# Kernel optimization log

Measured on AMD Instinct MI355X. Metric: run time of the kernel, lower is better.

Reference implementation:

```python
import jax, jax.numpy as jnp
import numpy as np

FILTER_1D = [1.0, 3.0, 3.0, 1.0]  # StyleGAN2 default resample filter
UP = 2


def make_kernel():
    f = jnp.array(FILTER_1D, dtype=jnp.float32)
    k = jnp.outer(f, f)
    k = k / jnp.sum(k)  # setup_filter normalization
    return k * (UP * UP)  # * 4 gain registered in the module


def setup_inputs() -> dict:
    key = jax.random.key(0)
    x = jax.random.normal(key, (4, 64, 256, 256), dtype=jnp.float32)
    return {"x": x, "kernel": make_kernel()}


def reference(x, kernel):
    # upfirdn2d(x, kernel, up=2): zero-insert upsample by 2, pad (fw+up-1)//2=2
    # before and (fw-up)//2=1 after, then FIR-convolve (true convolution ->
    # flip kernel; the [1,3,3,1] kernel is symmetric so this is a no-op, but
    # we flip for faithfulness). Implemented as a single depthwise dilated conv
    # so the padded/upsampled intermediate is never materialized.
    N, C, H, W = x.shape
    w = jnp.flip(kernel)[None, None, :, :].astype(x.dtype)  # [1,1,4,4]
    w = jnp.tile(w, (C, 1, 1, 1))  # depthwise weight [C,1,4,4]
    out = jax.lax.conv_general_dilated(
        x, w,
        window_strides=(1, 1),
        padding=((2, 1), (2, 1)),
        lhs_dilation=(UP, UP),
        dimension_numbers=("NCHW", "OIHW", "NCHW"),
        feature_group_count=C,
    )  # [N, C, 2H, 2W]
    return out
```

## Files before the change

kernel.cpp:

```cpp
#include <hip/hip_runtime.h>
#include <math.h>


template<int S>
__device__ __forceinline__ void hblend(float v0, float v1, float vm1,
                                       float vp0, float vp1, float q[4]) {
    if (S == 0) {
        q[0] = 0.25f*vm1 + 0.75f*v0;
        q[1] = 0.75f*v0  + 0.25f*v1;
        q[2] = 0.25f*v0  + 0.75f*v1;
        q[3] = 0.75f*v1  + 0.25f*vp0;
    } else if (S == 1) {
        q[0] = 0.75f*v0  + 0.25f*v1;
        q[1] = 0.25f*v0  + 0.75f*v1;
        q[2] = 0.75f*v1  + 0.25f*vp0;
        q[3] = 0.25f*v1  + 0.75f*vp0;
    } else if (S == 2) {
        q[0] = 0.25f*v0  + 0.75f*v1;
        q[1] = 0.75f*v1  + 0.25f*vp0;
        q[2] = 0.25f*v1  + 0.75f*vp0;
        q[3] = 0.75f*vp0 + 0.25f*vp1;
    } else {
        q[0] = 0.75f*v1  + 0.25f*vp0;
        q[1] = 0.25f*v1  + 0.75f*vp0;
        q[2] = 0.75f*vp0 + 0.25f*vp1;
        q[3] = 0.25f*vp0 + 0.75f*vp1;
    }
}

template<int S>
__device__ __forceinline__ void store_row(float* __restrict__ rp, int lane,
                                          int Wo, const float q1[4],
                                          const float q2[4],
                                          float v0lane, float v1lane) {
    *(float4*)(rp + S + 4 * lane) = make_float4(q1[0], q1[1], q1[2], q1[3]);
    int c0 = S + 256 + 4 * lane;
    if (c0 + 3 < Wo) {
        *(float4*)(rp + c0) = make_float4(q2[0], q2[1], q2[2], q2[3]);
    } else {
        if (c0     < Wo) rp[c0]     = q2[0];
        if (c0 + 1 < Wo) rp[c0 + 1] = q2[1];
        if (c0 + 2 < Wo) rp[c0 + 2] = q2[2];
        if (c0 + 3 < Wo) rp[c0 + 3] = q2[3];
    }
    if (S > 0 && lane == 0) {
        rp[0] = 0.75f * v0lane;
        if (S > 1) rp[1] = 0.75f * v0lane + 0.25f * v1lane;
        if (S > 2) rp[2] = 0.25f * v0lane + 0.75f * v1lane;
    }
}

template<int SE>
__device__ __forceinline__ void row_pair(
    const float* __restrict__ xp, float* __restrict__ out, size_t be,
    int lane, int i, int H, int W, int Ho, int Wo) {
    constexpr int SO = (SE + 1) & 3;
    int im = i > 0 ? i - 1 : 0;
    int ip = i < H - 1 ? i + 1 : H - 1;
    const float2* ra = (const float2*)(xp + im * W);
    const float2* rb = (const float2*)(xp + i  * W);
    const float2* rc = (const float2*)(xp + ip * W);
    float2 a1 = ra[lane],      b1 = rb[lane],      c1 = rc[lane];
    float2 a2 = ra[64 + lane], b2 = rb[64 + lane], c2 = rc[64 + lane];
    float w0 = (i > 0)     ? 0.25f : 0.0f;
    float wp = (i < H - 1) ? 0.25f : 0.0f;

    float ve10 = w0*a1.x + 0.75f*b1.x, ve11 = w0*a1.y + 0.75f*b1.y;
    float ve20 = w0*a2.x + 0.75f*b2.x, ve21 = w0*a2.y + 0.75f*b2.y;
    float vo10 = 0.75f*b1.x + wp*c1.x, vo11 = 0.75f*b1.y + wp*c1.y;
    float vo20 = 0.75f*b2.x + wp*c2.x, vo21 = 0.75f*b2.y + wp*c2.y;

    float t;
    float vm1e1 = __shfl_up(ve11, 1);   if (lane == 0)  vm1e1 = 0.f;
    float vp0e1 = __shfl_down(ve10, 1);
    t = __shfl(ve20, 0);                if (lane == 63) vp0e1 = t;
    float vp1e1 = __shfl_down(ve11, 1);
    t = __shfl(ve21, 0);                if (lane == 63) vp1e1 = t;
    float vm1e2 = __shfl_up(ve21, 1);
    t = __shfl(ve11, 63);               if (lane == 0)  vm1e2 = t;
    float vp0e2 = __shfl_down(ve20, 1); if (lane == 63) vp0e2 = 0.f;
    float vp1e2 = __shfl_down(ve21, 1); if (lane == 63) vp1e2 = 0.f;
    float vm1o1 = __shfl_up(vo11, 1);   if (lane == 0)  vm1o1 = 0.f;
    float vp0o1 = __shfl_down(vo10, 1);
    t = __shfl(vo20, 0);                if (lane == 63) vp0o1 = t;
    float vp1o1 = __shfl_down(vo11, 1);
    t = __shfl(vo21, 0);                if (lane == 63) vp1o1 = t;
    float vm1o2 = __shfl_up(vo21, 1);
    t = __shfl(vo11, 63);               if (lane == 0)  vm1o2 = t;
    float vp0o2 = __shfl_down(vo20, 1); if (lane == 63) vp0o2 = 0.f;
    float vp1o2 = __shfl_down(vo21, 1); if (lane == 63) vp1o2 = 0.f;

    float q1[4], q2[4];
    float* re = out + be;
    hblend<SE>(ve10, ve11, vm1e1, vp0e1, vp1e1, q1);
    hblend<SE>(ve20, ve21, vm1e2, vp0e2, vp1e2, q2);
    store_row<SE>(re, lane, Wo, q1, q2, ve10, ve11);

    if (2 * i + 1 < Ho) {
        float* ro = re + Wo;
        hblend<SO>(vo10, vo11, vm1o1, vp0o1, vp1o1, q1);
        hblend<SO>(vo20, vo21, vm1o2, vp0o2, vp1o2, q2);
        store_row<SO>(ro, lane, Wo, q1, q2, vo10, vo11);
    }
}

__global__ __launch_bounds__(256) void blur_up2_kernel(
    const float* __restrict__ x, float* __restrict__ out,
    int H, int W, int Ho, int Wo) {
    int lane = threadIdx.x;
    int i = blockIdx.y * 4 + threadIdx.y;
    int nc = blockIdx.z;
    if (i >= H) return;

    const float* xp = x + (size_t)nc * H * W;
    size_t be = (size_t)nc * Ho * Wo + (size_t)(2 * i) * Wo;
    int S = (int)((4 - (be & 3)) & 3);
    switch (S) {
        case 0:  row_pair<0>(xp, out, be, lane, i, H, W, Ho, Wo); break;
        case 1:  row_pair<1>(xp, out, be, lane, i, H, W, Ho, Wo); break;
        case 2:  row_pair<2>(xp, out, be, lane, i, H, W, Ho, Wo); break;
        default: row_pair<3>(xp, out, be, lane, i, H, W, Ho, Wo); break;
    }
}

extern "C" void kernel_launch(void* const* d_in, const int* in_sizes, int n_in,
                              void* d_out, int out_size, void* d_ws, size_t ws_size,
                              hipStream_t stream) {
    const float* x = (const float*)d_in[0];
    float* out = (float*)d_out;

    const int H = 256, W = 256;
    int NC = in_sizes[0] / (H * W);

    int hw_out = out_size / NC;
    int Wo = (int)(sqrt((double)hw_out) + 0.5);
    int Ho = hw_out / Wo;

    dim3 block(64, 4);
    dim3 grid(1, (H + 3) / 4, NC);
    blur_up2_kernel<<<grid, block, 0, stream>>>(x, out, H, W, Ho, Wo);
}
```

Measured before the change: 80.43 us.

## Process two input rows per thread and use nontemporal output stores

Each wavefront now handles two adjacent input rows, loading four input rows once and sharing the middle two between both output row pairs, which cuts redundant input reads from three to two rows per input row. The grid is halved to 32 row-blocks, and all output writes switch to nontemporal stores so the write-only output stream bypasses cache retention. The trade-off is fewer, heavier threads, which may reduce latency hiding. The grid size is now hardcoded for H=256.

Measured after the change: 82.96 us. 1.03x slower.

```diff
diff --git a/kernel.cpp b/kernel.cpp
--- a/kernel.cpp
+++ b/kernel.cpp
@@ -1,6 +1,8 @@
 #include <hip/hip_runtime.h>
 #include <math.h>
 
+
+typedef float vfloat4 __attribute__((ext_vector_type(4)));
 
 template<int S>
 __device__ __forceinline__ void hblend(float v0, float v1, float vm1,
@@ -33,37 +35,31 @@
                                           int Wo, const float q1[4],
                                           const float q2[4],
                                           float v0lane, float v1lane) {
-    *(float4*)(rp + S + 4 * lane) = make_float4(q1[0], q1[1], q1[2], q1[3]);
+    vfloat4 w1 = {q1[0], q1[1], q1[2], q1[3]};
+    __builtin_nontemporal_store(w1, (vfloat4*)(rp + S + 4 * lane));
     int c0 = S + 256 + 4 * lane;
     if (c0 + 3 < Wo) {
-        *(float4*)(rp + c0) = make_float4(q2[0], q2[1], q2[2], q2[3]);
+        vfloat4 w2 = {q2[0], q2[1], q2[2], q2[3]};
+        __builtin_nontemporal_store(w2, (vfloat4*)(rp + c0));
     } else {
-        if (c0     < Wo) rp[c0]     = q2[0];
-        if (c0 + 1 < Wo) rp[c0 + 1] = q2[1];
-        if (c0 + 2 < Wo) rp[c0 + 2] = q2[2];
-        if (c0 + 3 < Wo) rp[c0 + 3] = q2[3];
+        if (c0     < Wo) __builtin_nontemporal_store(q2[0], rp + c0);
+        if (c0 + 1 < Wo) __builtin_nontemporal_store(q2[1], rp + c0 + 1);
+        if (c0 + 2 < Wo) __builtin_nontemporal_store(q2[2], rp + c0 + 2);
+        if (c0 + 3 < Wo) __builtin_nontemporal_store(q2[3], rp + c0 + 3);
     }
     if (S > 0 && lane == 0) {
-        rp[0] = 0.75f * v0lane;
-        if (S > 1) rp[1] = 0.75f * v0lane + 0.25f * v1lane;
-        if (S > 2) rp[2] = 0.25f * v0lane + 0.75f * v1lane;
+        __builtin_nontemporal_store(0.75f * v0lane, rp);
+        if (S > 1) __builtin_nontemporal_store(0.75f * v0lane + 0.25f * v1lane, rp + 1);
+        if (S > 2) __builtin_nontemporal_store(0.25f * v0lane + 0.75f * v1lane, rp + 2);
     }
 }
 
 template<int SE>
-__device__ __forceinline__ void row_pair(
-    const float* __restrict__ xp, float* __restrict__ out, size_t be,
-    int lane, int i, int H, int W, int Ho, int Wo) {
+__device__ __forceinline__ void emit_pair(
+    float2 a1, float2 b1, float2 c1, float2 a2, float2 b2, float2 c2,
+    float w0, float wp, float* __restrict__ out, size_t be,
+    int lane, int orow, int Ho, int Wo) {
     constexpr int SO = (SE + 1) & 3;
-    int im = i > 0 ? i - 1 : 0;
-    int ip = i < H - 1 ? i + 1 : H - 1;
-    const float2* ra = (const float2*)(xp + im * W);
-    const float2* rb = (const float2*)(xp + i  * W);
-    const float2* rc = (const float2*)(xp + ip * W);
-    float2 a1 = ra[lane],      b1 = rb[lane],      c1 = rc[lane];
-    float2 a2 = ra[64 + lane], b2 = rb[64 + lane], c2 = rc[64 + lane];
-    float w0 = (i > 0)     ? 0.25f : 0.0f;
-    float wp = (i < H - 1) ? 0.25f : 0.0f;
 
     float ve10 = w0*a1.x + 0.75f*b1.x, ve11 = w0*a1.y + 0.75f*b1.y;
     float ve20 = w0*a2.x + 0.75f*b2.x, ve21 = w0*a2.y + 0.75f*b2.y;
@@ -96,7 +92,7 @@
     hblend<SE>(ve20, ve21, vm1e2, vp0e2, vp1e2, q2);
     store_row<SE>(re, lane, Wo, q1, q2, ve10, ve11);
 
-    if (2 * i + 1 < Ho) {
+    if (orow + 1 < Ho) {
         float* ro = re + Wo;
         hblend<SO>(vo10, vo11, vm1o1, vp0o1, vp1o1, q1);
         hblend<SO>(vo20, vo21, vm1o2, vp0o2, vp1o2, q2);
@@ -108,18 +104,46 @@
     const float* __restrict__ x, float* __restrict__ out,
     int H, int W, int Ho, int Wo) {
     int lane = threadIdx.x;
-    int i = blockIdx.y * 4 + threadIdx.y;
+    int r = blockIdx.y * 4 + threadIdx.y;
     int nc = blockIdx.z;
-    if (i >= H) return;
+    int i0 = 2 * r, i1 = 2 * r + 1;
 
     const float* xp = x + (size_t)nc * H * W;
-    size_t be = (size_t)nc * Ho * Wo + (size_t)(2 * i) * Wo;
-    int S = (int)((4 - (be & 3)) & 3);
-    switch (S) {
-        case 0:  row_pair<0>(xp, out, be, lane, i, H, W, Ho, Wo); break;
-        case 1:  row_pair<1>(xp, out, be, lane, i, H, W, Ho, Wo); break;
-        case 2:  row_pair<2>(xp, out, be, lane, i, H, W, Ho, Wo); break;
-        default: row_pair<3>(xp, out, be, lane, i, H, W, Ho, Wo); break;
+    const float2* prm = (const float2*)(xp + (i0 > 0 ? i0 - 1 : 0) * W);
+    const float2* pr0 = (const float2*)(xp + i0 * W);
+    const float2* pr1 = (const float2*)(xp + i1 * W);
+    const float2* prp = (const float2*)(xp + (i1 < H - 1 ? i1 + 1 : H - 1) * W);
+
+    float2 m1 = prm[lane], m2 = prm[64 + lane];
+    float2 z01 = pr0[lane], z02 = pr0[64 + lane];
+    float2 z11 = pr1[lane], z12 = pr1[64 + lane];
+    float2 p1 = prp[lane], p2 = prp[64 + lane];
+
+    float w_top = (i0 > 0)     ? 0.25f : 0.0f;
+    float w_bot = (i1 < H - 1) ? 0.25f : 0.0f;
+
+    size_t obase = (size_t)nc * Ho * Wo;
+    size_t be0 = obase + (size_t)(2 * i0) * Wo;
+    size_t be1 = be0 + 2 * (size_t)Wo;
+    int S0 = (int)((4 - (be0 & 3)) & 3);
+
+    switch (S0) {
+        case 0:
+            emit_pair<0>(m1, z01, z11, m2, z02, z12, w_top, 0.25f, out, be0, lane, 2*i0, Ho, Wo);
+            emit_pair<2>(z01, z11, p1, z02, z12, p2, 0.25f, w_bot, out, be1, lane, 2*i1, Ho, Wo);
+            break;
+        case 1:
+            emit_pair<1>(m1, z01, z11, m2, z02, z12, w_top, 0.25f, out, be0, lane, 2*i0, Ho, Wo);
+            emit_pair<3>(z01, z11, p1, z02, z12, p2, 0.25f, w_bot, out, be1, lane, 2*i1, Ho, Wo);
+            break;
+        case 2:
+            emit_pair<2>(m1, z01, z11, m2, z02, z12, w_top, 0.25f, out, be0, lane, 2*i0, Ho, Wo);
+            emit_pair<0>(z01, z11, p1, z02, z12, p2, 0.25f, w_bot, out, be1, lane, 2*i1, Ho, Wo);
+            break;
+        default:
+            emit_pair<3>(m1, z01, z11, m2, z02, z12, w_top, 0.25f, out, be0, lane, 2*i0, Ho, Wo);
+            emit_pair<1>(z01, z11, p1, z02, z12, p2, 0.25f, w_bot, out, be1, lane, 2*i1, Ho, Wo);
+            break;
     }
 }
 
@@ -137,6 +161,6 @@
     int Ho = hw_out / Wo;
 
     dim3 block(64, 4);
-    dim3 grid(1, (H + 3) / 4, NC);
+    dim3 grid(1, 32, NC);
     blur_up2_kernel<<<grid, block, 0, stream>>>(x, out, H, W, Ho, Wo);
 }
```

## Switch to persistent grid-stride kernel with one output row per wave

Applied to the files above, without the earlier changes.

Replaces the one-wave-per-input-row-pair mapping (each wave producing two output rows from three input rows) with a fixed grid of 2048 blocks, where each wave loops over single output rows in grid-stride order. Each iteration loads two input rows, blends them vertically, then interpolates horizontally with shuffles. The aim is to balance work across CUs and cut launch and tail overhead. The cost is more input-row loads per output row (two loads per output row instead of three per pair), which leans more on cache hits.

After: 105.1 us. 30.7% more time.

```diff
diff --git a/kernel.cpp b/kernel.cpp
--- a/kernel.cpp
+++ b/kernel.cpp
@@ -50,76 +50,75 @@
     }
 }
 
-template<int SE>
-__device__ __forceinline__ void row_pair(
-    const float* __restrict__ xp, float* __restrict__ out, size_t be,
-    int lane, int i, int H, int W, int Ho, int Wo) {
-    constexpr int SO = (SE + 1) & 3;
-    int im = i > 0 ? i - 1 : 0;
-    int ip = i < H - 1 ? i + 1 : H - 1;
-    const float2* ra = (const float2*)(xp + im * W);
-    const float2* rb = (const float2*)(xp + i  * W);
-    const float2* rc = (const float2*)(xp + ip * W);
-    float2 a1 = ra[lane],      b1 = rb[lane],      c1 = rc[lane];
-    float2 a2 = ra[64 + lane], b2 = rb[64 + lane], c2 = rc[64 + lane];
-    float w0 = (i > 0)     ? 0.25f : 0.0f;
-    float wp = (i < H - 1) ? 0.25f : 0.0f;
-
-    float ve10 = w0*a1.x + 0.75f*b1.x, ve11 = w0*a1.y + 0.75f*b1.y;
-    float ve20 = w0*a2.x + 0.75f*b2.x, ve21 = w0*a2.y + 0.75f*b2.y;
-    float vo10 = 0.75f*b1.x + wp*c1.x, vo11 = 0.75f*b1.y + wp*c1.y;
-    float vo20 = 0.75f*b2.x + wp*c2.x, vo21 = 0.75f*b2.y + wp*c2.y;
-
-    float t;
-    float vm1e1 = __shfl_up(ve11, 1);   if (lane == 0)  vm1e1 = 0.f;
-    float vp0e1 = __shfl_down(ve10, 1);
-    t = __shfl(ve20, 0);                if (lane == 63) vp0e1 = t;
-    float vp1e1 = __shfl_down(ve11, 1);
-    t = __shfl(ve21, 0);                if (lane == 63) vp1e1 = t;
-    float vm1e2 = __shfl_up(ve21, 1);
-    t = __shfl(ve11, 63);               if (lane == 0)  vm1e2 = t;
-    float vp0e2 = __shfl_down(ve20, 1); if (lane == 63) vp0e2 = 0.f;
-    float vp1e2 = __shfl_down(ve21, 1); if (lane == 63) vp1e2 = 0.f;
-    float vm1o1 = __shfl_up(vo11, 1);   if (lane == 0)  vm1o1 = 0.f;
-    float vp0o1 = __shfl_down(vo10, 1);
-    t = __shfl(vo20, 0);                if (lane == 63) vp0o1 = t;
-    float vp1o1 = __shfl_down(vo11, 1);
-    t = __shfl(vo21, 0);                if (lane == 63) vp1o1 = t;
-    float vm1o2 = __shfl_up(vo21, 1);
-    t = __shfl(vo11, 63);               if (lane == 0)  vm1o2 = t;
-    float vp0o2 = __shfl_down(vo20, 1); if (lane == 63) vp0o2 = 0.f;
-    float vp1o2 = __shfl_down(vo21, 1); if (lane == 63) vp1o2 = 0.f;
-
-    float q1[4], q2[4];
-    float* re = out + be;
-    hblend<SE>(ve10, ve11, vm1e1, vp0e1, vp1e1, q1);
-    hblend<SE>(ve20, ve21, vm1e2, vp0e2, vp1e2, q2);
-    store_row<SE>(re, lane, Wo, q1, q2, ve10, ve11);
-
-    if (2 * i + 1 < Ho) {
-        float* ro = re + Wo;
-        hblend<SO>(vo10, vo11, vm1o1, vp0o1, vp1o1, q1);
-        hblend<SO>(vo20, vo21, vm1o2, vp0o2, vp1o2, q2);
-        store_row<SO>(ro, lane, Wo, q1, q2, vo10, vo11);
-    }
-}
-
 __global__ __launch_bounds__(256) void blur_up2_kernel(
     const float* __restrict__ x, float* __restrict__ out,
-    int H, int W, int Ho, int Wo) {
+    int H, int W, int Ho, int Wo, int nrows, int nwaves) {
     int lane = threadIdx.x;
-    int i = blockIdx.y * 4 + threadIdx.y;
-    int nc = blockIdx.z;
-    if (i >= H) return;
+    int wid = blockIdx.x * 4 + threadIdx.y;
 
-    const float* xp = x + (size_t)nc * H * W;
-    size_t be = (size_t)nc * Ho * Wo + (size_t)(2 * i) * Wo;
-    int S = (int)((4 - (be & 3)) & 3);
-    switch (S) {
-        case 0:  row_pair<0>(xp, out, be, lane, i, H, W, Ho, Wo); break;
-        case 1:  row_pair<1>(xp, out, be, lane, i, H, W, Ho, Wo); break;
-        case 2:  row_pair<2>(xp, out, be, lane, i, H, W, Ho, Wo); break;
-        default: row_pair<3>(xp, out, be, lane, i, H, W, Ho, Wo); break;
+    int qd = nwaves / Ho, rd = nwaves - qd * Ho;
+    int ch = wid / Ho;
+    int c  = wid - ch * Ho;
+
+    for (int o = wid; o < nrows; o += nwaves) {
+        const float* xp = x + (size_t)ch * H * W;
+        int i = c >> 1;
+        bool even = (c & 1) == 0;
+        int ia = even ? i - 1 : i;
+        int ib = even ? i     : i + 1;
+        float wa = even ? 0.25f : 0.75f;
+        float wb = even ? 0.75f : 0.25f;
+        if (ia < 0)     { ia = 0;     wa = 0.f; }
+        if (ib > H - 1) { ib = H - 1; wb = 0.f; }
+
+        const float2* pa = (const float2*)(xp + ia * W);
+        const float2* pb = (const float2*)(xp + ib * W);
+        float2 a1 = pa[lane], a2 = pa[64 + lane];
+        float2 b1 = pb[lane], b2 = pb[64 + lane];
+
+        float v10 = wa * a1.x + wb * b1.x, v11 = wa * a1.y + wb * b1.y;
+        float v20 = wa * a2.x + wb * b2.x, v21 = wa * a2.y + wb * b2.y;
+
+        float t;
+        float vm11 = __shfl_up(v11, 1);   if (lane == 0)  vm11 = 0.f;
+        float vp01 = __shfl_down(v10, 1);
+        t = __shfl(v20, 0);               if (lane == 63) vp01 = t;
+        float vp11 = __shfl_down(v11, 1);
+        t = __shfl(v21, 0);               if (lane == 63) vp11 = t;
+        float vm12 = __shfl_up(v21, 1);
+        t = __shfl(v11, 63);              if (lane == 0)  vm12 = t;
+        float vp02 = __shfl_down(v20, 1); if (lane == 63) vp02 = 0.f;
+        float vp12 = __shfl_down(v21, 1); if (lane == 63) vp12 = 0.f;
+
+        size_t rbase = (size_t)ch * Ho * Wo + (size_t)c * Wo;
+        float* rp = out + rbase;
+        int S = (int)((4 - (rbase & 3)) & 3);
+        float q1[4], q2[4];
+        switch (S) {
+            case 0:
+                hblend<0>(v10, v11, vm11, vp01, vp11, q1);
+                hblend<0>(v20, v21, vm12, vp02, vp12, q2);
+                store_row<0>(rp, lane, Wo, q1, q2, v10, v11);
+                break;
+            case 1:
+                hblend<1>(v10, v11, vm11, vp01, vp11, q1);
+                hblend<1>(v20, v21, vm12, vp02, vp12, q2);
+                store_row<1>(rp, lane, Wo, q1, q2, v10, v11);
+                break;
+            case 2:
+                hblend<2>(v10, v11, vm11, vp01, vp11, q1);
+                hblend<2>(v20, v21, vm12, vp02, vp12, q2);
+                store_row<2>(rp, lane, Wo, q1, q2, v10, v11);
+                break;
+            default:
+                hblend<3>(v10, v11, vm11, vp01, vp11, q1);
+                hblend<3>(v20, v21, vm12, vp02, vp12, q2);
+                store_row<3>(rp, lane, Wo, q1, q2, v10, v11);
+                break;
+        }
+
+        ch += qd; c += rd;
+        if (c >= Ho) { c -= Ho; ++ch; }
     }
 }
 
@@ -136,7 +135,12 @@
     int Wo = (int)(sqrt((double)hw_out) + 0.5);
     int Ho = hw_out / Wo;
 
+    int nrows = NC * Ho;
+    int nblocks = 2048;
+    int nwaves = nblocks * 4;
+
     dim3 block(64, 4);
-    dim3 grid(1, (H + 3) / 4, NC);
-    blur_up2_kernel<<<grid, block, 0, stream>>>(x, out, H, W, Ho, Wo);
+    dim3 grid(nblocks);
+    blur_up2_kernel<<<grid, block, 0, stream>>>(x, out, H, W, Ho, Wo,
+                                                nrows, nwaves);
 }
```

## Process eight input rows per wave with a sliding register window

Applied to the files above, without the earlier changes.

Each wavefront now handles a strip of eight input rows instead of one, so the kernel needs far fewer blocks. The three-row vertical stencil is fed from a rolling window of registers, and two new rows are prefetched per step, so each input row is loaded about once per wave rather than three times across neighbouring waves. This cuts redundant global and L2 reads and gives each wave more independent memory work in flight. In exchange the grid is smaller and each thread uses more registers, which could lower occupancy.

New measurement: 79.85 us. Within noise of the previous version (-0.7%).

```diff
diff --git a/kernel.cpp b/kernel.cpp
--- a/kernel.cpp
+++ b/kernel.cpp
@@ -51,19 +51,11 @@
 }
 
 template<int SE>
-__device__ __forceinline__ void row_pair(
-    const float* __restrict__ xp, float* __restrict__ out, size_t be,
-    int lane, int i, int H, int W, int Ho, int Wo) {
+__device__ __forceinline__ void emit_pair(
+    float2 a1, float2 b1, float2 c1, float2 a2, float2 b2, float2 c2,
+    float w0, float wp, float* __restrict__ out, size_t be,
+    int lane, int orow, int Ho, int Wo) {
     constexpr int SO = (SE + 1) & 3;
-    int im = i > 0 ? i - 1 : 0;
-    int ip = i < H - 1 ? i + 1 : H - 1;
-    const float2* ra = (const float2*)(xp + im * W);
-    const float2* rb = (const float2*)(xp + i  * W);
-    const float2* rc = (const float2*)(xp + ip * W);
-    float2 a1 = ra[lane],      b1 = rb[lane],      c1 = rc[lane];
-    float2 a2 = ra[64 + lane], b2 = rb[64 + lane], c2 = rc[64 + lane];
-    float w0 = (i > 0)     ? 0.25f : 0.0f;
-    float wp = (i < H - 1) ? 0.25f : 0.0f;
 
     float ve10 = w0*a1.x + 0.75f*b1.x, ve11 = w0*a1.y + 0.75f*b1.y;
     float ve20 = w0*a2.x + 0.75f*b2.x, ve21 = w0*a2.y + 0.75f*b2.y;
@@ -96,7 +88,7 @@
     hblend<SE>(ve20, ve21, vm1e2, vp0e2, vp1e2, q2);
     store_row<SE>(re, lane, Wo, q1, q2, ve10, ve11);
 
-    if (2 * i + 1 < Ho) {
+    if (orow + 1 < Ho) {
         float* ro = re + Wo;
         hblend<SO>(vo10, vo11, vm1o1, vp0o1, vp1o1, q1);
         hblend<SO>(vo20, vo21, vm1o2, vp0o2, vp1o2, q2);
@@ -104,22 +96,62 @@
     }
 }
 
+__device__ __forceinline__ void ldrow(const float* __restrict__ xp, int row,
+                                      int lane, int W, float2& w1, float2& w2) {
+    const float2* p = (const float2*)(xp + row * W);
+    w1 = p[lane];
+    w2 = p[64 + lane];
+}
+
+template<int S0>
+__device__ __forceinline__ void run_wave(const float* __restrict__ xp,
+                                         float* __restrict__ out, size_t obase,
+                                         int rbase, int lane,
+                                         int H, int W, int Ho, int Wo) {
+    float2 A1, A2, B1, B2, C1, C2, D1, D2, E1, E2, F1, F2;
+    int r0 = rbase;
+    ldrow(xp, 2*r0 - 1 > 0 ? 2*r0 - 1 : 0, lane, W, A1, A2);
+    ldrow(xp, 2*r0,                        lane, W, B1, B2);
+    ldrow(xp, 2*r0 + 1,                    lane, W, C1, C2);
+    ldrow(xp, 2*r0 + 2 < H ? 2*r0 + 2 : H - 1, lane, W, D1, D2);
+
+#pragma unroll
+    for (int k = 0; k < 4; ++k) {
+        int rr = rbase + k;
+        if (k < 3) {
+            ldrow(xp, 2*rr + 3, lane, W, E1, E2);
+            ldrow(xp, 2*rr + 4 < H ? 2*rr + 4 : H - 1, lane, W, F1, F2);
+        }
+        float w_top = (rr > 0) ? 0.25f : 0.0f;
+        float w_bot = (2*rr + 1 < H - 1) ? 0.25f : 0.0f;
+        size_t be0 = obase + (size_t)(4 * rr) * Wo;
+        size_t be1 = be0 + 2 * (size_t)Wo;
+        emit_pair<S0>(A1, B1, C1, A2, B2, C2, w_top, 0.25f,
+                      out, be0, lane, 4 * rr, Ho, Wo);
+        emit_pair<(S0 + 2) & 3>(B1, C1, D1, B2, C2, D2, 0.25f, w_bot,
+                                out, be1, lane, 4 * rr + 2, Ho, Wo);
+        A1 = C1; A2 = C2; B1 = D1; B2 = D2;
+        C1 = E1; C2 = E2; D1 = F1; D2 = F2;
+    }
+}
+
 __global__ __launch_bounds__(256) void blur_up2_kernel(
     const float* __restrict__ x, float* __restrict__ out,
     int H, int W, int Ho, int Wo) {
     int lane = threadIdx.x;
-    int i = blockIdx.y * 4 + threadIdx.y;
-    int nc = blockIdx.z;
-    if (i >= H) return;
+    int w = blockIdx.x * 4 + threadIdx.y;
+    int ch = w >> 5;
+    int rbase = (w & 31) * 4;
 
-    const float* xp = x + (size_t)nc * H * W;
-    size_t be = (size_t)nc * Ho * Wo + (size_t)(2 * i) * Wo;
-    int S = (int)((4 - (be & 3)) & 3);
-    switch (S) {
-        case 0:  row_pair<0>(xp, out, be, lane, i, H, W, Ho, Wo); break;
-        case 1:  row_pair<1>(xp, out, be, lane, i, H, W, Ho, Wo); break;
-        case 2:  row_pair<2>(xp, out, be, lane, i, H, W, Ho, Wo); break;
-        default: row_pair<3>(xp, out, be, lane, i, H, W, Ho, Wo); break;
+    const float* xp = x + (size_t)ch * H * W;
+    size_t obase = (size_t)ch * Ho * Wo;
+    size_t be0 = obase + (size_t)(4 * rbase) * Wo;
+    int S0 = (int)((4 - (be0 & 3)) & 3);
+    switch (S0) {
+        case 0:  run_wave<0>(xp, out, obase, rbase, lane, H, W, Ho, Wo); break;
+        case 1:  run_wave<1>(xp, out, obase, rbase, lane, H, W, Ho, Wo); break;
+        case 2:  run_wave<2>(xp, out, obase, rbase, lane, H, W, Ho, Wo); break;
+        default: run_wave<3>(xp, out, obase, rbase, lane, H, W, Ho, Wo); break;
     }
 }
 
@@ -137,6 +169,6 @@
     int Ho = hw_out / Wo;
 
     dim3 block(64, 4);
-    dim3 grid(1, (H + 3) / 4, NC);
+    dim3 grid(NC * 8);
     blur_up2_kernel<<<grid, block, 0, stream>>>(x, out, H, W, Ho, Wo);
 }
```
